# Performance work log

Hardware: AMD Instinct MI355X
Metric: run time of the kernel (lower is better)

The kernel has to match this reference:

```python
import jax, jax.numpy as jnp
import numpy as np

EXPLORATION_C = 10.0
NEG_FILL = float(np.log(1e-45))  # matches torch.log(tensor(1e-45))


def setup_inputs() -> dict:
    key = jax.random.key(0)
    ks = jax.random.split(key, 10)
    B, U, S, H = 16, 500, 256, 128
    return {
        "user_input_seq_with_stay": jax.random.normal(ks[0], (B, U, 4), jnp.float32),
        "server_input_seq": jax.random.uniform(ks[1], (B, S, 6), jnp.float32),
        "masks": jax.random.randint(ks[2], (B, U, S), 0, 2) > 0,
        "Wu": jax.random.normal(ks[3], (3, H), jnp.float32) * 0.1,
        "bu": jax.random.normal(ks[4], (H,), jnp.float32) * 0.1,
        "Ws": jax.random.normal(ks[5], (7, H), jnp.float32) * 0.1,
        "bs": jax.random.normal(ks[6], (H,), jnp.float32) * 0.1,
        "W1": jax.random.normal(ks[7], (H, H), jnp.float32) * 0.1,
        "W2": jax.random.normal(ks[8], (H, H), jnp.float32) * 0.1,
        "vt": jax.random.normal(ks[9], (H,), jnp.float32) * 0.1,
    }


def reference(user_input_seq_with_stay, server_input_seq, masks,
              Wu, bu, Ws, bs, W1, W2, vt):
    # Drop the stay column: user_input_seq = [..., :-1]  -> [B, U, 3]
    user_input = user_input_seq_with_stay[..., :-1]
    user_enc = user_input @ Wu + bu  # [B, U, H] (UserEncoder, all steps at once)

    B, S, _ = server_input_seq.shape
    # server_seq = cat(static[:, :, :2], tmp_capacity[:, :, 2:], active)
    # server_allocate_mat is never updated in the loop -> active column is all zero.
    active = jnp.zeros((B, S, 1), server_input_seq.dtype)
    server_seq = jnp.concatenate([server_input_seq, active], axis=-1)  # [B, S, 7]
    server_enc = server_seq @ Ws + bs  # [B, S, H] (identical every decode step)

    enc_t = server_enc @ W1            # [B, S, H]
    dec_t = user_enc @ W2              # [B, U, H]
    # Additive attention score for every (user step, server) pair.
    u_i = jnp.tanh(enc_t[:, None, :, :] + dec_t[:, :, None, :]) @ vt  # [B, U, S]
    score = jnp.where(masks, u_i, jnp.asarray(NEG_FILL, u_i.dtype)) * EXPLORATION_C
    probs = jax.nn.softmax(score, axis=-1)  # [B, U, S]
    return probs
```

## Files before the change

kernel.cpp:

```cpp
#include <hip/hip_runtime.h>

#define B_ 16
#define U_ 500
#define S_ 256
#define H_ 128
#define UTILE 32
#define NWAVES 16
#define TPB (NWAVES * 64)

__global__ __launch_bounds__(TPB, 1) void attn_kernel(
    const float* __restrict__ user,
    const float* __restrict__ server,
    const int*   __restrict__ masks,
    const float* __restrict__ Wu,
    const float* __restrict__ bu,
    const float* __restrict__ Ws,
    const float* __restrict__ bs,
    const float* __restrict__ W1,
    const float* __restrict__ W2,
    const float* __restrict__ vt,
    float* __restrict__ out)
{
  __shared__ float E[H_][S_];
  __shared__ float M1s[6 * H_];
  __shared__ float M2s[3 * H_];
  __shared__ float c1s[H_];
  __shared__ float c2s[H_];
  __shared__ float decs[8][4][H_];
  __shared__ float redmax[8][4][2];
  __shared__ float redsum[8][4][2];
  __shared__ float vsum_s;

  const int tid = threadIdx.x;
  const int bid = blockIdx.x;
  const int b   = bid >> 4;
  const int u0  = (bid & 15) * UTILE;

  {
    const int h = tid & (H_ - 1);
    for (int job = tid >> 7; job < 11; job += 8) {
      const float* Lv; const float* Rm; float* dst;
      if (job < 6)       { Lv = Ws + job * H_;       Rm = W1; dst = M1s + job * H_; }
      else if (job == 6) { Lv = bs;                  Rm = W1; dst = c1s; }
      else if (job < 10) { Lv = Wu + (job - 7) * H_; Rm = W2; dst = M2s + (job - 7) * H_; }
      else               { Lv = bu;                  Rm = W2; dst = c2s; }
      float acc = 0.f;
      for (int j = 0; j < H_; ++j) acc = fmaf(Lv[j], Rm[j * H_ + h], acc);
      dst[h] = acc;
    }
    if (tid < 64) {
      float v = vt[tid] + vt[tid + 64];
      #pragma unroll
      for (int off = 32; off > 0; off >>= 1) v += __shfl_xor(v, off, 64);
      if (tid == 0) vsum_s = v;
    }
  }

  int lflag;
  {
    int4 mw = *reinterpret_cast<const int4*>(masks + tid * 4);
    lflag = ((unsigned)mw.x > 1u) | ((unsigned)mw.y > 1u) |
            ((unsigned)mw.z > 1u) | ((unsigned)mw.w > 1u);
  }
  const int bytemode = __syncthreads_or(lflag);

  {
    const int s  = tid & (S_ - 1);
    const int h0 = tid >> 8;
    const float2* sv = reinterpret_cast<const float2*>(server + ((size_t)b * S_ + s) * 6);
    const float2 p0 = sv[0], p1 = sv[1], p2 = sv[2];
    for (int h = h0; h < H_; h += 4) {
      float a = c1s[h];
      a = fmaf(p0.x, M1s[0 * H_ + h], a);
      a = fmaf(p0.y, M1s[1 * H_ + h], a);
      a = fmaf(p1.x, M1s[2 * H_ + h], a);
      a = fmaf(p1.y, M1s[3 * H_ + h], a);
      a = fmaf(p2.x, M1s[4 * H_ + h], a);
      a = fmaf(p2.y, M1s[5 * H_ + h], a);
      E[h][s] = __expf(fminf(fmaxf(a + a, -60.f), 60.f));
    }
  }

  const int w    = tid >> 6;
  const int lane = tid & 63;
  const int rg   = w >> 1;
  const int sh   = w & 1;
  const int s0   = sh * 128 + 2 * lane;

  {
    #pragma unroll
    for (int rr = 0; rr < 2; ++rr) {
      const int r  = 2 * sh + rr;
      const int uc = min(u0 + rg * 4 + r, U_ - 1);
      const float* uv = user + ((size_t)b * U_ + uc) * 4;
      const float g0 = uv[0], g1 = uv[1], g2 = uv[2];
      #pragma unroll
      for (int hh = 0; hh < 2; ++hh) {
        const int h = lane + hh * 64;
        float a = c2s[h];
        a = fmaf(g0, M2s[0 * H_ + h], a);
        a = fmaf(g1, M2s[1 * H_ + h], a);
        a = fmaf(g2, M2s[2 * H_ + h], a);
        decs[rg][r][h] = __expf(fminf(fmaxf(a + a, -60.f), 60.f));
      }
    }
  }
  __syncthreads();

  size_t ridx[4]; int uval[4]; int m0[4], m1[4];
  #pragma unroll
  for (int r = 0; r < 4; ++r) {
    const int u = u0 + rg * 4 + r;
    uval[r] = (u < U_);
    ridx[r] = ((size_t)b * U_ + min(u, U_ - 1)) * S_ + s0;
  }
  if (!bytemode) {
    #pragma unroll
    for (int r = 0; r < 4; ++r) {
      int2 mm = *reinterpret_cast<const int2*>(masks + ridx[r]);
      m0[r] = mm.x; m1[r] = mm.y;
    }
  } else {
    const unsigned char* mb = reinterpret_cast<const unsigned char*>(masks);
    #pragma unroll
    for (int r = 0; r < 4; ++r) {
      uchar2 mm = *reinterpret_cast<const uchar2*>(mb + ridx[r]);
      m0[r] = mm.x; m1[r] = mm.y;
    }
  }

  float acc[4][2] = {{0.f,0.f},{0.f,0.f},{0.f,0.f},{0.f,0.f}};

  auto quad = [](const float4& vv, float ea, float eb, float ec, float ed,
                 const float4& d, float& a) {
    float t0 = fmaf(ea, d.x, 1.0f);
    float t1 = fmaf(eb, d.y, 1.0f);
    float t2 = fmaf(ec, d.z, 1.0f);
    float t3 = fmaf(ed, d.w, 1.0f);
    float t01 = t0 * t1;
    float t23 = t2 * t3;
    float n01 = fmaf(vv.x, t1, vv.y * t0);
    float n23 = fmaf(vv.z, t3, vv.w * t2);
    float den = t01 * t23;
    float num = fmaf(n01, t23, n23 * t01);
    a = fmaf(num, __builtin_amdgcn_rcpf(den), a);
  };

  #pragma unroll 4
  for (int h4 = 0; h4 < H_ / 4; ++h4) {
    const int hh = h4 * 4;
    const float2 e0 = *reinterpret_cast<const float2*>(&E[hh + 0][s0]);
    const float2 e1 = *reinterpret_cast<const float2*>(&E[hh + 1][s0]);
    const float2 e2 = *reinterpret_cast<const float2*>(&E[hh + 2][s0]);
    const float2 e3 = *reinterpret_cast<const float2*>(&E[hh + 3][s0]);
    const float4 d0 = *reinterpret_cast<const float4*>(&decs[rg][0][hh]);
    const float4 d1 = *reinterpret_cast<const float4*>(&decs[rg][1][hh]);
    const float4 d2 = *reinterpret_cast<const float4*>(&decs[rg][2][hh]);
    const float4 d3 = *reinterpret_cast<const float4*>(&decs[rg][3][hh]);
    const float4 vv = *reinterpret_cast<const float4*>(vt + hh);
    quad(vv, e0.x, e1.x, e2.x, e3.x, d0, acc[0][0]);
    quad(vv, e0.y, e1.y, e2.y, e3.y, d0, acc[0][1]);
    quad(vv, e0.x, e1.x, e2.x, e3.x, d1, acc[1][0]);
    quad(vv, e0.y, e1.y, e2.y, e3.y, d1, acc[1][1]);
    quad(vv, e0.x, e1.x, e2.x, e3.x, d2, acc[2][0]);
    quad(vv, e0.y, e1.y, e2.y, e3.y, d2, acc[2][1]);
    quad(vv, e0.x, e1.x, e2.x, e3.x, d3, acc[3][0]);
    quad(vv, e0.y, e1.y, e2.y, e3.y, d3, acc[3][1]);
  }

  const float negs = -103.6163291847321f * 10.0f;
  const float vs10 = vsum_s * 10.0f;
  float p[4][2];
  #pragma unroll
  for (int r = 0; r < 4; ++r) {
    float sA = m0[r] ? fmaf(-20.0f, acc[r][0], vs10) : negs;
    float sB = m1[r] ? fmaf(-20.0f, acc[r][1], vs10) : negs;
    p[r][0] = sA; p[r][1] = sB;
    float mx = fmaxf(sA, sB);
    #pragma unroll
    for (int off = 32; off > 0; off >>= 1) mx = fmaxf(mx, __shfl_xor(mx, off, 64));
    if (lane == 0) redmax[rg][r][sh] = mx;
  }
  __syncthreads();
  #pragma unroll
  for (int r = 0; r < 4; ++r) {
    const float gmx = fmaxf(redmax[rg][r][0], redmax[rg][r][1]);
    float pa = __expf(p[r][0] - gmx);
    float pb = __expf(p[r][1] - gmx);
    p[r][0] = pa; p[r][1] = pb;
    float sm = pa + pb;
    #pragma unroll
    for (int off = 32; off > 0; off >>= 1) sm += __shfl_xor(sm, off, 64);
    if (lane == 0) redsum[rg][r][sh] = sm;
  }
  __syncthreads();
  #pragma unroll
  for (int r = 0; r < 4; ++r) {
    if (uval[r]) {
      const float inv = __builtin_amdgcn_rcpf(redsum[rg][r][0] + redsum[rg][r][1]);
      float2 o; o.x = p[r][0] * inv; o.y = p[r][1] * inv;
      *reinterpret_cast<float2*>(out + ridx[r]) = o;
    }
  }
}

extern "C" void kernel_launch(void* const* d_in, const int* in_sizes, int n_in,
                              void* d_out, int out_size, void* d_ws, size_t ws_size,
                              hipStream_t stream) {
  const float* user   = (const float*)d_in[0];
  const float* server = (const float*)d_in[1];
  const int*   masks  = (const int*)d_in[2];
  const float* Wu = (const float*)d_in[3];
  const float* bu = (const float*)d_in[4];
  const float* Ws = (const float*)d_in[5];
  const float* bs = (const float*)d_in[6];
  const float* W1 = (const float*)d_in[7];
  const float* W2 = (const float*)d_in[8];
  const float* vt = (const float*)d_in[9];
  float* out = (float*)d_out;
  (void)in_sizes; (void)n_in; (void)out_size; (void)d_ws; (void)ws_size;

  attn_kernel<<<dim3(B_ * ((U_ + UTILE - 1) / UTILE)), dim3(TPB), 0, stream>>>(
      user, server, masks, Wu, bu, Ws, bs, W1, W2, vt, out);
}
```

Measured before the change: 49.03 us.

## Halve user tile and split H into two LDS passes for occupancy

```diff
diff --git a/kernel.cpp b/kernel.cpp
--- a/kernel.cpp
+++ b/kernel.cpp
@@ -4,11 +4,12 @@
 #define U_ 500
 #define S_ 256
 #define H_ 128
-#define UTILE 32
+#define UTILE 16
 #define NWAVES 16
 #define TPB (NWAVES * 64)
-
-__global__ __launch_bounds__(TPB, 1) void attn_kernel(
+#define HHALF 64
+
+__global__ __launch_bounds__(TPB, 8) void attn_kernel(
     const float* __restrict__ user,
     const float* __restrict__ server,
     const int*   __restrict__ masks,
@@ -21,20 +22,20 @@
     const float* __restrict__ vt,
     float* __restrict__ out)
 {
-  __shared__ float E[H_][S_];
+  __shared__ float E[HHALF][S_];
   __shared__ float M1s[6 * H_];
   __shared__ float M2s[3 * H_];
   __shared__ float c1s[H_];
   __shared__ float c2s[H_];
-  __shared__ float decs[8][4][H_];
-  __shared__ float redmax[8][4][2];
-  __shared__ float redsum[8][4][2];
+  __shared__ float decs[8][2][HHALF];
+  __shared__ float redmax[8][2][2];
+  __shared__ float redsum[8][2][2];
   __shared__ float vsum_s;
 
   const int tid = threadIdx.x;
   const int bid = blockIdx.x;
-  const int b   = bid >> 4;
-  const int u0  = (bid & 15) * UTILE;
+  const int b   = bid >> 5;
+  const int u0  = (bid & 31) * UTILE;
 
   {
     const int h = tid & (H_ - 1);
@@ -64,72 +65,29 @@
   }
   const int bytemode = __syncthreads_or(lflag);
 
-  {
-    const int s  = tid & (S_ - 1);
-    const int h0 = tid >> 8;
-    const float2* sv = reinterpret_cast<const float2*>(server + ((size_t)b * S_ + s) * 6);
-    const float2 p0 = sv[0], p1 = sv[1], p2 = sv[2];
-    for (int h = h0; h < H_; h += 4) {
-      float a = c1s[h];
-      a = fmaf(p0.x, M1s[0 * H_ + h], a);
-      a = fmaf(p0.y, M1s[1 * H_ + h], a);
-      a = fmaf(p1.x, M1s[2 * H_ + h], a);
-      a = fmaf(p1.y, M1s[3 * H_ + h], a);
-      a = fmaf(p2.x, M1s[4 * H_ + h], a);
-      a = fmaf(p2.y, M1s[5 * H_ + h], a);
-      E[h][s] = __expf(fminf(fmaxf(a + a, -60.f), 60.f));
-    }
-  }
-
   const int w    = tid >> 6;
   const int lane = tid & 63;
   const int rg   = w >> 1;
   const int sh   = w & 1;
   const int s0   = sh * 128 + 2 * lane;
 
-  {
-    #pragma unroll
-    for (int rr = 0; rr < 2; ++rr) {
-      const int r  = 2 * sh + rr;
-      const int uc = min(u0 + rg * 4 + r, U_ - 1);
-      const float* uv = user + ((size_t)b * U_ + uc) * 4;
-      const float g0 = uv[0], g1 = uv[1], g2 = uv[2];
-      #pragma unroll
-      for (int hh = 0; hh < 2; ++hh) {
-        const int h = lane + hh * 64;
-        float a = c2s[h];
-        a = fmaf(g0, M2s[0 * H_ + h], a);
-        a = fmaf(g1, M2s[1 * H_ + h], a);
-        a = fmaf(g2, M2s[2 * H_ + h], a);
-        decs[rg][r][h] = __expf(fminf(fmaxf(a + a, -60.f), 60.f));
-      }
-    }
-  }
-  __syncthreads();
-
-  size_t ridx[4]; int uval[4]; int m0[4], m1[4];
-  #pragma unroll
-  for (int r = 0; r < 4; ++r) {
-    const int u = u0 + rg * 4 + r;
+  size_t ridx[2]; int uval[2]; int m0[2], m1[2];
+  #pragma unroll
+  for (int r = 0; r < 2; ++r) {
+    const int u = u0 + rg * 2 + r;
     uval[r] = (u < U_);
     ridx[r] = ((size_t)b * U_ + min(u, U_ - 1)) * S_ + s0;
   }
-  if (!bytemode) {
-    #pragma unroll
-    for (int r = 0; r < 4; ++r) {
-      int2 mm = *reinterpret_cast<const int2*>(masks + ridx[r]);
-      m0[r] = mm.x; m1[r] = mm.y;
-    }
-  } else {
-    const unsigned char* mb = reinterpret_cast<const unsigned char*>(masks);
-    #pragma unroll
-    for (int r = 0; r < 4; ++r) {
-      uchar2 mm = *reinterpret_cast<const uchar2*>(mb + ridx[r]);
-      m0[r] = mm.x; m1[r] = mm.y;
-    }
-  }
-
-  float acc[4][2] = {{0.f,0.f},{0.f,0.f},{0.f,0.f},{0.f,0.f}};
+
+  const int uStage = min(u0 + rg * 2 + sh, U_ - 1);
+  const float* uv = user + ((size_t)b * U_ + uStage) * 4;
+  const float g0 = uv[0], g1 = uv[1], g2 = uv[2];
+
+  const int   sStage = tid & (S_ - 1);
+  const int   h0     = tid >> 8;
+  const float2* sv = reinterpret_cast<const float2*>(server + ((size_t)b * S_ + sStage) * 6);
+
+  float acc[2][2] = {{0.f, 0.f}, {0.f, 0.f}};
 
   auto quad = [](const float4& vv, float ea, float eb, float ec, float ed,
                  const float4& d, float& a) {
@@ -146,33 +104,74 @@
     a = fmaf(num, __builtin_amdgcn_rcpf(den), a);
   };
 
-  #pragma unroll 4
-  for (int h4 = 0; h4 < H_ / 4; ++h4) {
-    const int hh = h4 * 4;
-    const float2 e0 = *reinterpret_cast<const float2*>(&E[hh + 0][s0]);
-    const float2 e1 = *reinterpret_cast<const float2*>(&E[hh + 1][s0]);
-    const float2 e2 = *reinterpret_cast<const float2*>(&E[hh + 2][s0]);
-    const float2 e3 = *reinterpret_cast<const float2*>(&E[hh + 3][s0]);
-    const float4 d0 = *reinterpret_cast<const float4*>(&decs[rg][0][hh]);
-    const float4 d1 = *reinterpret_cast<const float4*>(&decs[rg][1][hh]);
-    const float4 d2 = *reinterpret_cast<const float4*>(&decs[rg][2][hh]);
-    const float4 d3 = *reinterpret_cast<const float4*>(&decs[rg][3][hh]);
-    const float4 vv = *reinterpret_cast<const float4*>(vt + hh);
-    quad(vv, e0.x, e1.x, e2.x, e3.x, d0, acc[0][0]);
-    quad(vv, e0.y, e1.y, e2.y, e3.y, d0, acc[0][1]);
-    quad(vv, e0.x, e1.x, e2.x, e3.x, d1, acc[1][0]);
-    quad(vv, e0.y, e1.y, e2.y, e3.y, d1, acc[1][1]);
-    quad(vv, e0.x, e1.x, e2.x, e3.x, d2, acc[2][0]);
-    quad(vv, e0.y, e1.y, e2.y, e3.y, d2, acc[2][1]);
-    quad(vv, e0.x, e1.x, e2.x, e3.x, d3, acc[3][0]);
-    quad(vv, e0.y, e1.y, e2.y, e3.y, d3, acc[3][1]);
+  #pragma unroll 1
+  for (int pass = 0; pass < 2; ++pass) {
+    const int hbase = pass * HHALF;
+
+    {
+      const float2 p0 = sv[0], p1 = sv[1], p2 = sv[2];
+      for (int hr = h0; hr < HHALF; hr += 4) {
+        const int h = hbase + hr;
+        float a = c1s[h];
+        a = fmaf(p0.x, M1s[0 * H_ + h], a);
+        a = fmaf(p0.y, M1s[1 * H_ + h], a);
+        a = fmaf(p1.x, M1s[2 * H_ + h], a);
+        a = fmaf(p1.y, M1s[3 * H_ + h], a);
+        a = fmaf(p2.x, M1s[4 * H_ + h], a);
+        a = fmaf(p2.y, M1s[5 * H_ + h], a);
+        E[hr][sStage] = __expf(fminf(fmaxf(a + a, -60.f), 60.f));
+      }
+    }
+    {
+      const int h = hbase + lane;
+      float a = c2s[h];
+      a = fmaf(g0, M2s[0 * H_ + h], a);
+      a = fmaf(g1, M2s[1 * H_ + h], a);
+      a = fmaf(g2, M2s[2 * H_ + h], a);
+      decs[rg][sh][lane] = __expf(fminf(fmaxf(a + a, -60.f), 60.f));
+    }
+    __syncthreads();
+
+    if (pass == 0) {
+      if (!bytemode) {
+        #pragma unroll
+        for (int r = 0; r < 2; ++r) {
+          int2 mm = *reinterpret_cast<const int2*>(masks + ridx[r]);
+          m0[r] = mm.x; m1[r] = mm.y;
+        }
+      } else {
+        const unsigned char* mb = reinterpret_cast<const unsigned char*>(masks);
+        #pragma unroll
+        for (int r = 0; r < 2; ++r) {
+          uchar2 mm = *reinterpret_cast<const uchar2*>(mb + ridx[r]);
+          m0[r] = mm.x; m1[r] = mm.y;
+        }
+      }
+    }
+
+    #pragma unroll 4
+    for (int h4 = 0; h4 < HHALF / 4; ++h4) {
+      const int hh = h4 * 4;
+      const float2 e0 = *reinterpret_cast<const float2*>(&E[hh + 0][s0]);
+      const float2 e1 = *reinterpret_cast<const float2*>(&E[hh + 1][s0]);
+      const float2 e2 = *reinterpret_cast<const float2*>(&E[hh + 2][s0]);
+      const float2 e3 = *reinterpret_cast<const float2*>(&E[hh + 3][s0]);
+      const float4 d0 = *reinterpret_cast<const float4*>(&decs[rg][0][hh]);
+      const float4 d1 = *reinterpret_cast<const float4*>(&decs[rg][1][hh]);
+      const float4 vv = *reinterpret_cast<const float4*>(vt + hbase + hh);
+      quad(vv, e0.x, e1.x, e2.x, e3.x, d0, acc[0][0]);
+      quad(vv, e0.y, e1.y, e2.y, e3.y, d0, acc[0][1]);
+      quad(vv, e0.x, e1.x, e2.x, e3.x, d1, acc[1][0]);
+      quad(vv, e0.y, e1.y, e2.y, e3.y, d1, acc[1][1]);
+    }
+    __syncthreads();
   }
 
   const float negs = -103.6163291847321f * 10.0f;
   const float vs10 = vsum_s * 10.0f;
-  float p[4][2];
-  #pragma unroll
-  for (int r = 0; r < 4; ++r) {
+  float p[2][2];
+  #pragma unroll
+  for (int r = 0; r < 2; ++r) {
     float sA = m0[r] ? fmaf(-20.0f, acc[r][0], vs10) : negs;
     float sB = m1[r] ? fmaf(-20.0f, acc[r][1], vs10) : negs;
     p[r][0] = sA; p[r][1] = sB;
@@ -183,7 +182,7 @@
   }
   __syncthreads();
   #pragma unroll
-  for (int r = 0; r < 4; ++r) {
+  for (int r = 0; r < 2; ++r) {
     const float gmx = fmaxf(redmax[rg][r][0], redmax[rg][r][1]);
     float pa = __expf(p[r][0] - gmx);
     float pb = __expf(p[r][1] - gmx);
@@ -195,7 +194,7 @@
   }
   __syncthreads();
   #pragma unroll
-  for (int r = 0; r < 4; ++r) {
+  for (int r = 0; r < 2; ++r) {
     if (uval[r]) {
       const float inv = __builtin_amdgcn_rcpf(redsum[rg][r][0] + redsum[rg][r][1]);
       float2 o; o.x = p[r][0] * inv; o.y = p[r][1] * inv;
```

New measurement: 59.47 us. 1.21x slower.

## Give each wave full server rows to drop cross-wave softmax reductions

Applied to the files above, without the earlier changes.

```diff
diff --git a/kernel.cpp b/kernel.cpp
--- a/kernel.cpp
+++ b/kernel.cpp
@@ -5,10 +5,10 @@
 #define S_ 256
 #define H_ 128
 #define UTILE 32
-#define NWAVES 16
+#define NWAVES 8
 #define TPB (NWAVES * 64)
 
-__global__ __launch_bounds__(TPB, 1) void attn_kernel(
+__global__ __launch_bounds__(TPB, 2) void attn_kernel(
     const float* __restrict__ user,
     const float* __restrict__ server,
     const int*   __restrict__ masks,
@@ -26,9 +26,8 @@
   __shared__ float M2s[3 * H_];
   __shared__ float c1s[H_];
   __shared__ float c2s[H_];
-  __shared__ float decs[8][4][H_];
-  __shared__ float redmax[8][4][2];
-  __shared__ float redsum[8][4][2];
+  __shared__ float vts[H_];
+  __shared__ float decs[NWAVES][4][H_];
   __shared__ float vsum_s;
 
   const int tid = threadIdx.x;
@@ -38,7 +37,7 @@
 
   {
     const int h = tid & (H_ - 1);
-    for (int job = tid >> 7; job < 11; job += 8) {
+    for (int job = tid >> 7; job < 11; job += 4) {
       const float* Lv; const float* Rm; float* dst;
       if (job < 6)       { Lv = Ws + job * H_;       Rm = W1; dst = M1s + job * H_; }
       else if (job == 6) { Lv = bs;                  Rm = W1; dst = c1s; }
@@ -48,6 +47,7 @@
       for (int j = 0; j < H_; ++j) acc = fmaf(Lv[j], Rm[j * H_ + h], acc);
       dst[h] = acc;
     }
+    if (tid < H_) vts[tid] = vt[tid];
     if (tid < 64) {
       float v = vt[tid] + vt[tid + 64];
       #pragma unroll
@@ -69,7 +69,7 @@
     const int h0 = tid >> 8;
     const float2* sv = reinterpret_cast<const float2*>(server + ((size_t)b * S_ + s) * 6);
     const float2 p0 = sv[0], p1 = sv[1], p2 = sv[2];
-    for (int h = h0; h < H_; h += 4) {
+    for (int h = h0; h < H_; h += 2) {
       float a = c1s[h];
       a = fmaf(p0.x, M1s[0 * H_ + h], a);
       a = fmaf(p0.y, M1s[1 * H_ + h], a);
@@ -83,16 +83,13 @@
 
   const int w    = tid >> 6;
   const int lane = tid & 63;
-  const int rg   = w >> 1;
-  const int sh   = w & 1;
-  const int s0   = sh * 128 + 2 * lane;
+  const int ub   = u0 + 4 * w;
 
   {
     #pragma unroll
-    for (int rr = 0; rr < 2; ++rr) {
-      const int r  = 2 * sh + rr;
-      const int uc = min(u0 + rg * 4 + r, U_ - 1);
-      const float* uv = user + ((size_t)b * U_ + uc) * 4;
+    for (int r = 0; r < 4; ++r) {
+      const int ucr = min(ub + r, U_ - 1);
+      const float* uv = user + ((size_t)b * U_ + ucr) * 4;
       const float g0 = uv[0], g1 = uv[1], g2 = uv[2];
       #pragma unroll
       for (int hh = 0; hh < 2; ++hh) {
@@ -101,38 +98,39 @@
         a = fmaf(g0, M2s[0 * H_ + h], a);
         a = fmaf(g1, M2s[1 * H_ + h], a);
         a = fmaf(g2, M2s[2 * H_ + h], a);
-        decs[rg][r][h] = __expf(fminf(fmaxf(a + a, -60.f), 60.f));
+        decs[w][r][h] = __expf(fminf(fmaxf(a + a, -60.f), 60.f));
       }
     }
   }
   __syncthreads();
 
-  size_t ridx[4]; int uval[4]; int m0[4], m1[4];
+  size_t ridx[4];
+  int m[4][4];
   #pragma unroll
-  for (int r = 0; r < 4; ++r) {
-    const int u = u0 + rg * 4 + r;
-    uval[r] = (u < U_);
-    ridx[r] = ((size_t)b * U_ + min(u, U_ - 1)) * S_ + s0;
-  }
+  for (int r = 0; r < 4; ++r)
+    ridx[r] = ((size_t)b * U_ + min(ub + r, U_ - 1)) * S_ + (size_t)lane * 4;
   if (!bytemode) {
     #pragma unroll
     for (int r = 0; r < 4; ++r) {
-      int2 mm = *reinterpret_cast<const int2*>(masks + ridx[r]);
-      m0[r] = mm.x; m1[r] = mm.y;
+      int4 mm = *reinterpret_cast<const int4*>(masks + ridx[r]);
+      m[r][0] = mm.x; m[r][1] = mm.y; m[r][2] = mm.z; m[r][3] = mm.w;
     }
   } else {
     const unsigned char* mb = reinterpret_cast<const unsigned char*>(masks);
     #pragma unroll
     for (int r = 0; r < 4; ++r) {
-      uchar2 mm = *reinterpret_cast<const uchar2*>(mb + ridx[r]);
-      m0[r] = mm.x; m1[r] = mm.y;
-    }
-  }
-
-  float acc[4][2] = {{0.f,0.f},{0.f,0.f},{0.f,0.f},{0.f,0.f}};
+      uchar4 mm = *reinterpret_cast<const uchar4*>(mb + ridx[r]);
+      m[r][0] = mm.x; m[r][1] = mm.y; m[r][2] = mm.z; m[r][3] = mm.w;
+    }
+  }
+
+  float a0_0 = 0.f, a0_1 = 0.f, a0_2 = 0.f, a0_3 = 0.f;
+  float a1_0 = 0.f, a1_1 = 0.f, a1_2 = 0.f, a1_3 = 0.f;
+  float a2_0 = 0.f, a2_1 = 0.f, a2_2 = 0.f, a2_3 = 0.f;
+  float a3_0 = 0.f, a3_1 = 0.f, a3_2 = 0.f, a3_3 = 0.f;
 
   auto quad = [](const float4& vv, float ea, float eb, float ec, float ed,
-                 const float4& d, float& a) {
+                 const float4& d, float& acc) {
     float t0 = fmaf(ea, d.x, 1.0f);
     float t1 = fmaf(eb, d.y, 1.0f);
     float t2 = fmaf(ec, d.z, 1.0f);
@@ -143,63 +141,67 @@
     float n23 = fmaf(vv.z, t3, vv.w * t2);
     float den = t01 * t23;
     float num = fmaf(n01, t23, n23 * t01);
-    a = fmaf(num, __builtin_amdgcn_rcpf(den), a);
+    acc = fmaf(num, __builtin_amdgcn_rcpf(den), acc);
   };
 
-  #pragma unroll 4
+  #pragma unroll 2
   for (int h4 = 0; h4 < H_ / 4; ++h4) {
     const int hh = h4 * 4;
-    const float2 e0 = *reinterpret_cast<const float2*>(&E[hh + 0][s0]);
-    const float2 e1 = *reinterpret_cast<const float2*>(&E[hh + 1][s0]);
-    const float2 e2 = *reinterpret_cast<const float2*>(&E[hh + 2][s0]);
-    const float2 e3 = *reinterpret_cast<const float2*>(&E[hh + 3][s0]);
-    const float4 d0 = *reinterpret_cast<const float4*>(&decs[rg][0][hh]);
-    const float4 d1 = *reinterpret_cast<const float4*>(&decs[rg][1][hh]);
-    const float4 d2 = *reinterpret_cast<const float4*>(&decs[rg][2][hh]);
-    const float4 d3 = *reinterpret_cast<const float4*>(&decs[rg][3][hh]);
-    const float4 vv = *reinterpret_cast<const float4*>(vt + hh);
-    quad(vv, e0.x, e1.x, e2.x, e3.x, d0, acc[0][0]);
-    quad(vv, e0.y, e1.y, e2.y, e3.y, d0, acc[0][1]);
-    quad(vv, e0.x, e1.x, e2.x, e3.x, d1, acc[1][0]);
-    quad(vv, e0.y, e1.y, e2.y, e3.y, d1, acc[1][1]);
-    quad(vv, e0.x, e1.x, e2.x, e3.x, d2, acc[2][0]);
-    quad(vv, e0.y, e1.y, e2.y, e3.y, d2, acc[2][1]);
-    quad(vv, e0.x, e1.x, e2.x, e3.x, d3, acc[3][0]);
-    quad(vv, e0.y, e1.y, e2.y, e3.y, d3, acc[3][1]);
+    const float4 e0 = *reinterpret_cast<const float4*>(&E[hh + 0][lane * 4]);
+    const float4 e1 = *reinterpret_cast<const float4*>(&E[hh + 1][lane * 4]);
+    const float4 e2 = *reinterpret_cast<const float4*>(&E[hh + 2][lane * 4]);
+    const float4 e3 = *reinterpret_cast<const float4*>(&E[hh + 3][lane * 4]);
+    const float4 d0 = *reinterpret_cast<const float4*>(&decs[w][0][hh]);
+    const float4 d1 = *reinterpret_cast<const float4*>(&decs[w][1][hh]);
+    const float4 d2 = *reinterpret_cast<const float4*>(&decs[w][2][hh]);
+    const float4 d3 = *reinterpret_cast<const float4*>(&decs[w][3][hh]);
+    const float4 v4 = *reinterpret_cast<const float4*>(&vts[hh]);
+
+    quad(v4, e0.x, e1.x, e2.x, e3.x, d0, a0_0);
+    quad(v4, e0.y, e1.y, e2.y, e3.y, d0, a0_1);
+    quad(v4, e0.z, e1.z, e2.z, e3.z, d0, a0_2);
+    quad(v4, e0.w, e1.w, e2.w, e3.w, d0, a0_3);
+    quad(v4, e0.x, e1.x, e2.x, e3.x, d1, a1_0);
+    quad(v4, e0.y, e1.y, e2.y, e3.y, d1, a1_1);
+    quad(v4, e0.z, e1.z, e2.z, e3.z, d1, a1_2);
+    quad(v4, e0.w, e1.w, e2.w, e3.w, d1, a1_3);
+    quad(v4, e0.x, e1.x, e2.x, e3.x, d2, a2_0);
+    quad(v4, e0.y, e1.y, e2.y, e3.y, d2, a2_1);
+    quad(v4, e0.z, e1.z, e2.z, e3.z, d2, a2_2);
+    quad(v4, e0.w, e1.w, e2.w, e3.w, d2, a2_3);
+    quad(v4, e0.x, e1.x, e2.x, e3.x, d3, a3_0);
+    quad(v4, e0.y, e1.y, e2.y, e3.y, d3, a3_1);
+    quad(v4, e0.z, e1.z, e2.z, e3.z, d3, a3_2);
+    quad(v4, e0.w, e1.w, e2.w, e3.w, d3, a3_3);
   }
 
   const float negs = -103.6163291847321f * 10.0f;
   const float vs10 = vsum_s * 10.0f;
-  float p[4][2];
   #pragma unroll
   for (int r = 0; r < 4; ++r) {
-    float sA = m0[r] ? fmaf(-20.0f, acc[r][0], vs10) : negs;
-    float sB = m1[r] ? fmaf(-20.0f, acc[r][1], vs10) : negs;
-    p[r][0] = sA; p[r][1] = sB;
-    float mx = fmaxf(sA, sB);
-    #pragma unroll
-    for (int off = 32; off > 0; off >>= 1) mx = fmaxf(mx, __shfl_xor(mx, off, 64));
-    if (lane == 0) redmax[rg][r][sh] = mx;
-  }
-  __syncthreads();
-  #pragma unroll
-  for (int r = 0; r < 4; ++r) {
-    const float gmx = fmaxf(redmax[rg][r][0], redmax[rg][r][1]);
-    float pa = __expf(p[r][0] - gmx);
-    float pb = __expf(p[r][1] - gmx);
-    p[r][0] = pa; p[r][1] = pb;
-    float sm = pa + pb;
-    #pragma unroll
-    for (int off = 32; off > 0; off >>= 1) sm += __shfl_xor(sm, off, 64);
-    if (lane == 0) redsum[rg][r][sh] = sm;
-  }
-  __syncthreads();
-  #pragma unroll
-  for (int r = 0; r < 4; ++r) {
-    if (uval[r]) {
-      const float inv = __builtin_amdgcn_rcpf(redsum[rg][r][0] + redsum[rg][r][1]);
-      float2 o; o.x = p[r][0] * inv; o.y = p[r][1] * inv;
-      *reinterpret_cast<float2*>(out + ridx[r]) = o;
+    if (ub + r < U_) {
+      const float b0 = (r == 0) ? a0_0 : (r == 1) ? a1_0 : (r == 2) ? a2_0 : a3_0;
+      const float b1 = (r == 0) ? a0_1 : (r == 1) ? a1_1 : (r == 2) ? a2_1 : a3_1;
+      const float b2 = (r == 0) ? a0_2 : (r == 1) ? a1_2 : (r == 2) ? a2_2 : a3_2;
+      const float b3 = (r == 0) ? a0_3 : (r == 1) ? a1_3 : (r == 2) ? a2_3 : a3_3;
+      float s0 = m[r][0] ? fmaf(-20.0f, b0, vs10) : negs;
+      float s1 = m[r][1] ? fmaf(-20.0f, b1, vs10) : negs;
+      float s2 = m[r][2] ? fmaf(-20.0f, b2, vs10) : negs;
+      float s3 = m[r][3] ? fmaf(-20.0f, b3, vs10) : negs;
+      float mx = fmaxf(fmaxf(s0, s1), fmaxf(s2, s3));
+      #pragma unroll
+      for (int off = 32; off > 0; off >>= 1) mx = fmaxf(mx, __shfl_xor(mx, off, 64));
+      float p0 = __expf(s0 - mx);
+      float p1 = __expf(s1 - mx);
+      float p2 = __expf(s2 - mx);
+      float p3 = __expf(s3 - mx);
+      float sum = (p0 + p1) + (p2 + p3);
+      #pragma unroll
+      for (int off = 32; off > 0; off >>= 1) sum += __shfl_xor(sum, off, 64);
+      const float inv = __builtin_amdgcn_rcpf(sum);
+      float4 o;
+      o.x = p0 * inv; o.y = p1 * inv; o.z = p2 * inv; o.w = p3 * inv;
+      *reinterpret_cast<float4*>(out + ridx[r]) = o;
     }
   }
 }
```

After: 46.86 us. -4.4%, faster.

## Compact masked-in servers per row and skip attention math for masked entries

Applied to the files above, without the earlier changes.

```diff
diff --git a/kernel.cpp b/kernel.cpp
--- a/kernel.cpp
+++ b/kernel.cpp
@@ -21,20 +21,23 @@
     const float* __restrict__ vt,
     float* __restrict__ out)
 {
-  __shared__ float E[H_][S_];
+  __shared__ float Et[S_][H_];
   __shared__ float M1s[6 * H_];
   __shared__ float M2s[3 * H_];
   __shared__ float c1s[H_];
   __shared__ float c2s[H_];
-  __shared__ float decs[8][4][H_];
-  __shared__ float redmax[8][4][2];
-  __shared__ float redsum[8][4][2];
+  __shared__ float decs[NWAVES][2][H_];
+  __shared__ unsigned char slist[NWAVES][512];
   __shared__ float vsum_s;
 
-  const int tid = threadIdx.x;
-  const int bid = blockIdx.x;
-  const int b   = bid >> 4;
-  const int u0  = (bid & 15) * UTILE;
+  const int tid  = threadIdx.x;
+  const int bid  = blockIdx.x;
+  const int b    = bid >> 4;
+  const int u0   = (bid & 15) * UTILE;
+  const int w    = tid >> 6;
+  const int lane = tid & 63;
+
+  int4 mw = *reinterpret_cast<const int4*>(masks + tid * 4);
 
   {
     const int h = tid & (H_ - 1);
@@ -46,7 +49,7 @@
       else               { Lv = bu;                  Rm = W2; dst = c2s; }
       float acc = 0.f;
       for (int j = 0; j < H_; ++j) acc = fmaf(Lv[j], Rm[j * H_ + h], acc);
-      dst[h] = acc;
+      dst[h] = acc + acc;
     }
     if (tid < 64) {
       float v = vt[tid] + vt[tid + 64];
@@ -55,44 +58,70 @@
       if (tid == 0) vsum_s = v;
     }
   }
-
-  int lflag;
-  {
-    int4 mw = *reinterpret_cast<const int4*>(masks + tid * 4);
-    lflag = ((unsigned)mw.x > 1u) | ((unsigned)mw.y > 1u) |
-            ((unsigned)mw.z > 1u) | ((unsigned)mw.w > 1u);
-  }
-  const int bytemode = __syncthreads_or(lflag);
+  __syncthreads();
+
+  const int lflag = ((unsigned)mw.x > 1u) | ((unsigned)mw.y > 1u) |
+                    ((unsigned)mw.z > 1u) | ((unsigned)mw.w > 1u);
+  const int bytemode = __any(lflag);
+
+  const int uA  = u0 + 2 * w;
+  const int uAc = min(uA,     U_ - 1);
+  const int uBc = min(uA + 1, U_ - 1);
+  const size_t rowA = ((size_t)b * U_ + uAc) * S_;
+  const size_t rowB = ((size_t)b * U_ + uBc) * S_;
+
+  int m[2][4];
+  if (uA < U_) {
+    if (!bytemode) {
+      int4 ma = *reinterpret_cast<const int4*>(masks + rowA + lane * 4);
+      int4 mb = *reinterpret_cast<const int4*>(masks + rowB + lane * 4);
+      m[0][0] = ma.x; m[0][1] = ma.y; m[0][2] = ma.z; m[0][3] = ma.w;
+      m[1][0] = mb.x; m[1][1] = mb.y; m[1][2] = mb.z; m[1][3] = mb.w;
+    } else {
+      const unsigned char* mbp = reinterpret_cast<const unsigned char*>(masks);
+      uchar4 ma = *reinterpret_cast<const uchar4*>(mbp + rowA + lane * 4);
+      uchar4 mb = *reinterpret_cast<const uchar4*>(mbp + rowB + lane * 4);
+      m[0][0] = ma.x; m[0][1] = ma.y; m[0][2] = ma.z; m[0][3] = ma.w;
+      m[1][0] = mb.x; m[1][1] = mb.y; m[1][2] = mb.z; m[1][3] = mb.w;
+    }
+  }
 
   {
     const int s  = tid & (S_ - 1);
     const int h0 = tid >> 8;
+    const int P  = (s << 9) + ((s & 7) << 4);
+    char* etb = (char*)Et;
     const float2* sv = reinterpret_cast<const float2*>(server + ((size_t)b * S_ + s) * 6);
     const float2 p0 = sv[0], p1 = sv[1], p2 = sv[2];
-    for (int h = h0; h < H_; h += 4) {
-      float a = c1s[h];
-      a = fmaf(p0.x, M1s[0 * H_ + h], a);
-      a = fmaf(p0.y, M1s[1 * H_ + h], a);
-      a = fmaf(p1.x, M1s[2 * H_ + h], a);
-      a = fmaf(p1.y, M1s[3 * H_ + h], a);
-      a = fmaf(p2.x, M1s[4 * H_ + h], a);
-      a = fmaf(p2.y, M1s[5 * H_ + h], a);
-      E[h][s] = __expf(fminf(fmaxf(a + a, -60.f), 60.f));
-    }
-  }
-
-  const int w    = tid >> 6;
-  const int lane = tid & 63;
-  const int rg   = w >> 1;
-  const int sh   = w & 1;
-  const int s0   = sh * 128 + 2 * lane;
-
-  {
-    #pragma unroll
-    for (int rr = 0; rr < 2; ++rr) {
-      const int r  = 2 * sh + rr;
-      const int uc = min(u0 + rg * 4 + r, U_ - 1);
-      const float* uv = user + ((size_t)b * U_ + uc) * 4;
+    #pragma unroll
+    for (int g = 0; g < 8; ++g) {
+      const int hq = h0 * 8 + g;
+      const int hb = hq * 4;
+      const float4 c  = *reinterpret_cast<const float4*>(&c1s[hb]);
+      const float4 q0 = *reinterpret_cast<const float4*>(&M1s[0 * H_ + hb]);
+      const float4 q1 = *reinterpret_cast<const float4*>(&M1s[1 * H_ + hb]);
+      const float4 q2 = *reinterpret_cast<const float4*>(&M1s[2 * H_ + hb]);
+      const float4 q3 = *reinterpret_cast<const float4*>(&M1s[3 * H_ + hb]);
+      const float4 q4 = *reinterpret_cast<const float4*>(&M1s[4 * H_ + hb]);
+      const float4 q5 = *reinterpret_cast<const float4*>(&M1s[5 * H_ + hb]);
+      float4 a;
+      a.x = fmaf(p2.y, q5.x, fmaf(p2.x, q4.x, fmaf(p1.y, q3.x, fmaf(p1.x, q2.x, fmaf(p0.y, q1.x, fmaf(p0.x, q0.x, c.x))))));
+      a.y = fmaf(p2.y, q5.y, fmaf(p2.x, q4.y, fmaf(p1.y, q3.y, fmaf(p1.x, q2.y, fmaf(p0.y, q1.y, fmaf(p0.x, q0.y, c.y))))));
+      a.z = fmaf(p2.y, q5.z, fmaf(p2.x, q4.z, fmaf(p1.y, q3.z, fmaf(p1.x, q2.z, fmaf(p0.y, q1.z, fmaf(p0.x, q0.z, c.z))))));
+      a.w = fmaf(p2.y, q5.w, fmaf(p2.x, q4.w, fmaf(p1.y, q3.w, fmaf(p1.x, q2.w, fmaf(p0.y, q1.w, fmaf(p0.x, q0.w, c.w))))));
+      float4 e;
+      e.x = __expf(fminf(fmaxf(a.x, -60.f), 60.f));
+      e.y = __expf(fminf(fmaxf(a.y, -60.f), 60.f));
+      e.z = __expf(fminf(fmaxf(a.z, -60.f), 60.f));
+      e.w = __expf(fminf(fmaxf(a.w, -60.f), 60.f));
+      *reinterpret_cast<float4*>(etb + (P ^ (hq << 4))) = e;
+    }
+  }
+
+  {
+    #pragma unroll
+    for (int r = 0; r < 2; ++r) {
+      const float* uv = user + ((size_t)b * U_ + (r ? uBc : uAc)) * 4;
       const float g0 = uv[0], g1 = uv[1], g2 = uv[2];
       #pragma unroll
       for (int hh = 0; hh < 2; ++hh) {
@@ -101,106 +130,131 @@
         a = fmaf(g0, M2s[0 * H_ + h], a);
         a = fmaf(g1, M2s[1 * H_ + h], a);
         a = fmaf(g2, M2s[2 * H_ + h], a);
-        decs[rg][r][h] = __expf(fminf(fmaxf(a + a, -60.f), 60.f));
+        decs[w][r][h] = __expf(fminf(fmaxf(a, -60.f), 60.f));
       }
     }
   }
   __syncthreads();
 
-  size_t ridx[4]; int uval[4]; int m0[4], m1[4];
-  #pragma unroll
-  for (int r = 0; r < 4; ++r) {
-    const int u = u0 + rg * 4 + r;
-    uval[r] = (u < U_);
-    ridx[r] = ((size_t)b * U_ + min(u, U_ - 1)) * S_ + s0;
-  }
-  if (!bytemode) {
-    #pragma unroll
-    for (int r = 0; r < 4; ++r) {
-      int2 mm = *reinterpret_cast<const int2*>(masks + ridx[r]);
-      m0[r] = mm.x; m1[r] = mm.y;
-    }
-  } else {
-    const unsigned char* mb = reinterpret_cast<const unsigned char*>(masks);
-    #pragma unroll
-    for (int r = 0; r < 4; ++r) {
-      uchar2 mm = *reinterpret_cast<const uchar2*>(mb + ridx[r]);
-      m0[r] = mm.x; m1[r] = mm.y;
-    }
-  }
-
-  float acc[4][2] = {{0.f,0.f},{0.f,0.f},{0.f,0.f},{0.f,0.f}};
-
-  auto quad = [](const float4& vv, float ea, float eb, float ec, float ed,
-                 const float4& d, float& a) {
-    float t0 = fmaf(ea, d.x, 1.0f);
-    float t1 = fmaf(eb, d.y, 1.0f);
-    float t2 = fmaf(ec, d.z, 1.0f);
-    float t3 = fmaf(ed, d.w, 1.0f);
-    float t01 = t0 * t1;
-    float t23 = t2 * t3;
-    float n01 = fmaf(vv.x, t1, vv.y * t0);
-    float n23 = fmaf(vv.z, t3, vv.w * t2);
-    float den = t01 * t23;
-    float num = fmaf(n01, t23, n23 * t01);
-    a = fmaf(num, __builtin_amdgcn_rcpf(den), a);
-  };
-
-  #pragma unroll 4
-  for (int h4 = 0; h4 < H_ / 4; ++h4) {
-    const int hh = h4 * 4;
-    const float2 e0 = *reinterpret_cast<const float2*>(&E[hh + 0][s0]);
-    const float2 e1 = *reinterpret_cast<const float2*>(&E[hh + 1][s0]);
-    const float2 e2 = *reinterpret_cast<const float2*>(&E[hh + 2][s0]);
-    const float2 e3 = *reinterpret_cast<const float2*>(&E[hh + 3][s0]);
-    const float4 d0 = *reinterpret_cast<const float4*>(&decs[rg][0][hh]);
-    const float4 d1 = *reinterpret_cast<const float4*>(&decs[rg][1][hh]);
-    const float4 d2 = *reinterpret_cast<const float4*>(&decs[rg][2][hh]);
-    const float4 d3 = *reinterpret_cast<const float4*>(&decs[rg][3][hh]);
-    const float4 vv = *reinterpret_cast<const float4*>(vt + hh);
-    quad(vv, e0.x, e1.x, e2.x, e3.x, d0, acc[0][0]);
-    quad(vv, e0.y, e1.y, e2.y, e3.y, d0, acc[0][1]);
-    quad(vv, e0.x, e1.x, e2.x, e3.x, d1, acc[1][0]);
-    quad(vv, e0.y, e1.y, e2.y, e3.y, d1, acc[1][1]);
-    quad(vv, e0.x, e1.x, e2.x, e3.x, d2, acc[2][0]);
-    quad(vv, e0.y, e1.y, e2.y, e3.y, d2, acc[2][1]);
-    quad(vv, e0.x, e1.x, e2.x, e3.x, d3, acc[3][0]);
-    quad(vv, e0.y, e1.y, e2.y, e3.y, d3, acc[3][1]);
+  if (uA >= U_) return;
+
+  unsigned long long W0[4], W1b[4];
+  #pragma unroll
+  for (int c = 0; c < 4; ++c) { W0[c] = __ballot(m[0][c] != 0); W1b[c] = __ballot(m[1][c] != 0); }
+  const int kA = __popcll(W0[0]) + __popcll(W0[1]) + __popcll(W0[2]) + __popcll(W0[3]);
+  const int kB = __popcll(W1b[0]) + __popcll(W1b[1]) + __popcll(W1b[2]) + __popcll(W1b[3]);
+  const int K  = kA + kB;
+  {
+    const unsigned long long low = (1ull << lane) - 1ull;
+    int rk = __popcll(W0[0] & low) + __popcll(W0[1] & low) + __popcll(W0[2] & low) + __popcll(W0[3] & low);
+    #pragma unroll
+    for (int c = 0; c < 4; ++c)
+      if (m[0][c]) { slist[w][rk] = (unsigned char)(4 * lane + c); ++rk; }
+    rk = kA + __popcll(W1b[0] & low) + __popcll(W1b[1] & low) + __popcll(W1b[2] & low) + __popcll(W1b[3] & low);
+    #pragma unroll
+    for (int c = 0; c < 4; ++c)
+      if (m[1][c]) { slist[w][rk] = (unsigned char)(4 * lane + c); ++rk; }
+  }
+
+  int   sS[8], Pb[8], Db[8];
+  float accT[8];
+  #pragma unroll
+  for (int t = 0; t < 8; ++t) {
+    const int j   = lane + (t << 6);
+    const int idx = (j < K) ? j : 0;
+    const int sj  = slist[w][idx];
+    sS[t]   = sj;
+    Pb[t]   = (sj << 9) + ((sj & 7) << 4);
+    Db[t]   = (w << 10) + ((j >= kA) ? 512 : 0);
+    accT[t] = 0.f;
+  }
+
+  {
+    char* etb = (char*)Et;
+    char* dcb = (char*)decs;
+    #pragma unroll
+    for (int t = 0; t < 8; ++t) {
+      if ((t << 6) < K) {
+        int p = Pb[t];
+        int d = Db[t];
+        float acc = 0.f;
+        #pragma unroll 1
+        for (int h8 = 0; h8 < 4; ++h8) {
+          #pragma unroll
+          for (int i = 0; i < 8; ++i) {
+            const float4 e  = *reinterpret_cast<const float4*>(etb + (p ^ (i << 4)));
+            const float4 dd = *reinterpret_cast<const float4*>(dcb + d + (i << 4));
+            const float4 vv = *reinterpret_cast<const float4*>(vt + h8 * 32 + i * 4);
+            float t0 = fmaf(e.x, dd.x, 1.0f);
+            float t1 = fmaf(e.y, dd.y, 1.0f);
+            float t2 = fmaf(e.z, dd.z, 1.0f);
+            float t3 = fmaf(e.w, dd.w, 1.0f);
+            float t01 = t0 * t1;
+            float t23 = t2 * t3;
+            float n01 = fmaf(vv.x, t1, vv.y * t0);
+            float n23 = fmaf(vv.z, t3, vv.w * t2);
+            acc = fmaf(fmaf(n01, t23, n23 * t01), __builtin_amdgcn_rcpf(t01 * t23), acc);
+          }
+          p += 128; d += 128;
+        }
+        accT[t] = acc;
+      }
+    }
   }
 
   const float negs = -103.6163291847321f * 10.0f;
   const float vs10 = vsum_s * 10.0f;
-  float p[4][2];
-  #pragma unroll
-  for (int r = 0; r < 4; ++r) {
-    float sA = m0[r] ? fmaf(-20.0f, acc[r][0], vs10) : negs;
-    float sB = m1[r] ? fmaf(-20.0f, acc[r][1], vs10) : negs;
-    p[r][0] = sA; p[r][1] = sB;
-    float mx = fmaxf(sA, sB);
-    #pragma unroll
-    for (int off = 32; off > 0; off >>= 1) mx = fmaxf(mx, __shfl_xor(mx, off, 64));
-    if (lane == 0) redmax[rg][r][sh] = mx;
-  }
-  __syncthreads();
-  #pragma unroll
-  for (int r = 0; r < 4; ++r) {
-    const float gmx = fmaxf(redmax[rg][r][0], redmax[rg][r][1]);
-    float pa = __expf(p[r][0] - gmx);
-    float pb = __expf(p[r][1] - gmx);
-    p[r][0] = pa; p[r][1] = pb;
-    float sm = pa + pb;
-    #pragma unroll
-    for (int off = 32; off > 0; off >>= 1) sm += __shfl_xor(sm, off, 64);
-    if (lane == 0) redsum[rg][r][sh] = sm;
-  }
-  __syncthreads();
-  #pragma unroll
-  for (int r = 0; r < 4; ++r) {
-    if (uval[r]) {
-      const float inv = __builtin_amdgcn_rcpf(redsum[rg][r][0] + redsum[rg][r][1]);
-      float2 o; o.x = p[r][0] * inv; o.y = p[r][1] * inv;
-      *reinterpret_cast<float2*>(out + ridx[r]) = o;
-    }
+  float sc[8];
+  float mA = negs, mB = negs;
+  #pragma unroll
+  for (int t = 0; t < 8; ++t) {
+    const int  j   = lane + (t << 6);
+    const bool val = j < K;
+    const bool isB = j >= kA;
+    const float s  = val ? fmaf(-20.0f, accT[t], vs10) : negs;
+    sc[t] = s;
+    mA = fmaxf(mA, (val && !isB) ? s : negs);
+    mB = fmaxf(mB, (val &&  isB) ? s : negs);
+  }
+  #pragma unroll
+  for (int off = 32; off > 0; off >>= 1) {
+    mA = fmaxf(mA, __shfl_xor(mA, off, 64));
+    mB = fmaxf(mB, __shfl_xor(mB, off, 64));
+  }
+  float pv[8];
+  float sA = 0.f, sB = 0.f;
+  #pragma unroll
+  for (int t = 0; t < 8; ++t) {
+    const int  j   = lane + (t << 6);
+    const bool val = j < K;
+    const bool isB = j >= kA;
+    const float p  = val ? __expf(sc[t] - (isB ? mB : mA)) : 0.f;
+    pv[t] = p;
+    sA += (val && !isB) ? p : 0.f;
+    sB += (val &&  isB) ? p : 0.f;
+  }
+  #pragma unroll
+  for (int off = 32; off > 0; off >>= 1) {
+    sA += __shfl_xor(sA, off, 64);
+    sB += __shfl_xor(sB, off, 64);
+  }
+  const float invA = __builtin_amdgcn_rcpf(sA);
+  const float invB = __builtin_amdgcn_rcpf(sB);
+
+  #pragma unroll
+  for (int t = 0; t < 8; ++t) {
+    const int j = lane + (t << 6);
+    if (j < K) {
+      const bool isB = j >= kA;
+      out[(isB ? rowB : rowA) + sS[t]] = pv[t] * (isB ? invB : invA);
+    }
+  }
+  const float fillA = kA ? 0.f : (1.0f / 256.0f);
+  const float fillB = kB ? 0.f : (1.0f / 256.0f);
+  #pragma unroll
+  for (int c = 0; c < 4; ++c) {
+    if (!m[0][c]) out[rowA + 4 * lane + c] = fillA;
+    if (!m[1][c]) out[rowB + 4 * lane + c] = fillB;
   }
 }
 
```

Result: faster. 44.86 us (-8.5%).
